# Performance work log

Measured on AMD Instinct MI355X. Metric: run time of the kernel, lower is better.

## Reference

```python
import jax, jax.numpy as jnp
import numpy as np
from jax import lax

D = 512        # datapathSize (= slow-net hidden size = embedding size)
H = 20         # nonlinearAfterSlowHiddenSize
V = 32000      # softmaxOutputHeadSize = xEmbeddingsNum
T = 1024       # sequence length (number of sequential fast-weight updates)


def setup_inputs() -> dict:
    key = jax.random.key(0)
    ks = jax.random.split(key, 12)
    inp = {}
    inp["tokens"] = jax.random.randint(ks[0], (T,), 0, V)
    inp["targets"] = jax.random.randint(ks[1], (T,), 0, V)
    # learned parameters
    inp["embed"] = jax.random.normal(ks[2], (V, D), dtype=jnp.float32)
    # fastWeightsInit = rand(D,D) * (1/D)
    inp["fw_init"] = jax.random.uniform(ks[3], (D, D), dtype=jnp.float32) * (1.0 / D)
    inp["eta"] = jnp.array(1.0, dtype=jnp.float32)
    inp["wa"] = jax.random.normal(ks[4], (D, D), dtype=jnp.float32) * 0.05
    inp["wb"] = jax.random.normal(ks[5], (D, D), dtype=jnp.float32) * 0.05
    # nonlinearAfterSlow: Linear(D,H) -> selu -> Linear(H,D); stored as (in,out)
    lim_a = 1.0 / np.sqrt(D)
    inp["mlp_aw"] = jax.random.uniform(ks[6], (D, H), dtype=jnp.float32, minval=-lim_a, maxval=lim_a)
    inp["mlp_ab"] = jax.random.uniform(ks[7], (H,), dtype=jnp.float32, minval=-lim_a, maxval=lim_a)
    lim_b = 1.0 / np.sqrt(H)
    inp["mlp_bw"] = jax.random.uniform(ks[8], (H, D), dtype=jnp.float32, minval=-lim_b, maxval=lim_b)
    inp["mlp_bb"] = jax.random.uniform(ks[9], (D,), dtype=jnp.float32, minval=-lim_b, maxval=lim_b)
    # logit head Linear(D, V)
    inp["head_w"] = jax.random.uniform(ks[10], (D, V), dtype=jnp.float32, minval=-lim_a, maxval=lim_a)
    inp["head_b"] = jax.random.uniform(ks[11], (V,), dtype=jnp.float32, minval=-lim_a, maxval=lim_a)
    return inp


def reference(tokens, targets, embed, fw_init, eta, wa, wb,
              mlp_aw, mlp_ab, mlp_bw, mlp_bb, head_w, head_b):
    xs = embed[tokens]  # [T, D]

    def step(fw, x):
        # SlowNetB.forwardAndUpdate for one token
        z0 = x @ wa                      # [D]
        z1 = x @ wb                      # [D]
        fw_new = jnp.tanh(fw + eta * jnp.outer(z0, z1))  # [D, D]
        y = x @ fw_new                   # [D]
        return fw_new, y

    _, ys = lax.scan(step, fw_init, xs)  # ys: [T, D]

    # NonlinearLayer (batched over T)
    h = jax.nn.selu(ys @ mlp_aw + mlp_ab) @ mlp_bw + mlp_bb  # [T, D]
    mixed = 0.5 * h + 0.5 * xs
    logits = mixed @ head_w + head_b     # [T, V]

    logp = jax.nn.log_softmax(logits, axis=-1)
    loss = -jnp.mean(jnp.take_along_axis(logp, targets[:, None], axis=1))
    return logits, loss
```

## Files before the change

### kernel.cpp

```cpp
#include <hip/hip_runtime.h>

#define D 512
#define H 20
#define V 32000
#define T 1024

typedef unsigned int uint;
typedef __attribute__((ext_vector_type(8))) short short8;
typedef __attribute__((ext_vector_type(4))) float floatx4;

__device__ __forceinline__ unsigned short f2bf(float f) {
    unsigned u = __builtin_bit_cast(unsigned, f);
    u += 0x7fffu + ((u >> 16) & 1u);
    return (unsigned short)(u >> 16);
}

template <int CTRL>
__device__ __forceinline__ float dpp_add(float v) {
    int x = __builtin_amdgcn_update_dpp(0, __builtin_bit_cast(int, v), CTRL, 0xf, 0xf, true);
    return v + __builtin_bit_cast(float, x);
}
__device__ __forceinline__ float reduce16(float v) {
    v = dpp_add<0xB1>(v);
    v = dpp_add<0x4E>(v);
    v = dpp_add<0x141>(v);
    v = dpp_add<0x140>(v);
    return v;
}

__global__ __launch_bounds__(256) void gather_kernel(const int* __restrict__ tokens,
                                                     const float* __restrict__ embed,
                                                     float* __restrict__ xs) {
    int idx = blockIdx.x * 256 + threadIdx.x;
    int row = idx >> 7;
    int c   = idx & 127;
    float4 v = ((const float4*)(embed + (long)tokens[row] * D))[c];
    ((float4*)xs)[idx] = v;
}

__global__ __launch_bounds__(256) void zgemm_kernel(const float* __restrict__ xs,
                                                    const float* __restrict__ wa,
                                                    const float* __restrict__ wb,
                                                    float* __restrict__ z0,
                                                    float* __restrict__ z1) {
    __shared__ float Xs[16 * 36];
    __shared__ float Ws[16 * 68];
    const int tid = threadIdx.x;
    const int n0 = blockIdx.x * 64, m0 = blockIdx.y * 32;
    const float* Wm = blockIdx.z ? wb : wa;
    float* Z = blockIdx.z ? z1 : z0;
    const int tx = tid & 15, ty = tid >> 4;
    const int xr = tid >> 3, xk = (tid & 7) * 2;
    const int wr = tid >> 4, wc = (tid & 15) * 4;
    float acc[2][4] = {};
    for (int k0 = 0; k0 < D; k0 += 16) {
        float2 xv = *(const float2*)(xs + (m0 + xr) * D + k0 + xk);
        float4 wv = *(const float4*)(Wm + (k0 + wr) * D + n0 + wc);
        Xs[(xk + 0) * 36 + xr] = xv.x;
        Xs[(xk + 1) * 36 + xr] = xv.y;
        *(float4*)(Ws + wr * 68 + wc) = wv;
        __syncthreads();
#pragma unroll
        for (int k = 0; k < 16; k++) {
            float a0 = Xs[k * 36 + 2 * ty];
            float a1 = Xs[k * 36 + 2 * ty + 1];
            float4 b = *(const float4*)(Ws + k * 68 + tx * 4);
            float bv[4] = {b.x, b.y, b.z, b.w};
#pragma unroll
            for (int c = 0; c < 4; c++) {
                acc[0][c] = __builtin_fmaf(a0, bv[c], acc[0][c]);
                acc[1][c] = __builtin_fmaf(a1, bv[c], acc[1][c]);
            }
        }
        __syncthreads();
    }
    float4 v0 = {acc[0][0], acc[0][1], acc[0][2], acc[0][3]};
    float4 v1 = {acc[1][0], acc[1][1], acc[1][2], acc[1][3]};
    *(float4*)(Z + (m0 + 2 * ty + 0) * D + n0 + tx * 4) = v0;
    *(float4*)(Z + (m0 + 2 * ty + 1) * D + n0 + tx * 4) = v1;
}

#define CC 2.8853900817779268f

#define LOADC(ZA, ZB, XA, XB, EC, tbase)                       \
    _Pragma("unroll")                                          \
    for (int c = 0; c < 8; c++) {                              \
        int tr = (tbase + c) * D;                              \
        ZA[c] = z0[tr + i0];                                   \
        ZB[c] = z0[tr + i1];                                   \
        XA[c] = xs[tr + i0];                                   \
        XB[c] = xs[tr + i1];                                   \
        EC[c] = z1[tr + j] * ETAC;                             \
    }

#define COMPUTE(ZA, ZB, XA, XB, EC, tbase)                     \
    {                                                          \
        float p[8];                                            \
        _Pragma("unroll")                                      \
        for (int c = 0; c < 8; c++) {                          \
            float e = EC[c];                                   \
            float e0 = __builtin_amdgcn_exp2f(__builtin_fmaf(e, ZA[c], g0)); \
            float e1 = __builtin_amdgcn_exp2f(__builtin_fmaf(e, ZB[c], g1)); \
            float r0 = __builtin_amdgcn_rcpf(e0 + 1.0f);       \
            float r1 = __builtin_amdgcn_rcpf(e1 + 1.0f);       \
            g0 = __builtin_fmaf(-2.0f * CC, r0, CC);           \
            g1 = __builtin_fmaf(-2.0f * CC, r1, CC);           \
            p[c] = XA[c] * g0 + XB[c] * g1;                    \
        }                                                      \
        _Pragma("unroll")                                      \
        for (int c = 0; c < 8; c++) {                          \
            float v = reduce16(p[c]);                          \
            v += __shfl_xor(v, 16, 64);                        \
            v += __shfl_xor(v, 32, 64);                        \
            p[c] = v;                                          \
        }                                                      \
        if (lane == 0) {                                       \
            _Pragma("unroll")                                  \
            for (int c = 0; c < 8; c++) yp[(tbase + c) * D] = p[c]; \
        }                                                      \
    }

__global__ __launch_bounds__(64) void scan_kernel(const float* __restrict__ z0,
                                                  const float* __restrict__ z1,
                                                  const float* __restrict__ xs,
                                                  const float* __restrict__ fw_init,
                                                  const float* __restrict__ eta_p,
                                                  float* __restrict__ ypart) {
    const int lane = threadIdx.x;
    const int bid = blockIdx.x;
    const int j = bid & 511;
    const int q = bid >> 9;
    const int i0 = q * 128 + lane;
    const int i1 = i0 + 64;
    const float eta = *eta_p;
    const float ETAC = eta * CC;
    float g0 = CC * fw_init[(long)i0 * D + j];
    float g1 = CC * fw_init[(long)i1 * D + j];
    float* yp = ypart + (long)q * T * D + j;

    float zaA[8], zbA[8], xaA[8], xbA[8], ecA[8];
    float zaB[8], zbB[8], xaB[8], xbB[8], ecB[8];
    LOADC(zaA, zbA, xaA, xbA, ecA, 0);
    for (int t0 = 0; t0 < T; t0 += 16) {
        LOADC(zaB, zbB, xaB, xbB, ecB, t0 + 8);
        COMPUTE(zaA, zbA, xaA, xbA, ecA, t0);
        if (t0 + 16 < T) { LOADC(zaA, zbA, xaA, xbA, ecA, t0 + 16); }
        COMPUTE(zaB, zbB, xaB, xbB, ecB, t0 + 8);
    }
}

__global__ __launch_bounds__(256) void mlp_fused_kernel(const float* __restrict__ ypart,
                                                        const float* __restrict__ xs,
                                                        const float* __restrict__ Aw,
                                                        const float* __restrict__ Ab,
                                                        const float* __restrict__ Bw,
                                                        const float* __restrict__ Bb,
                                                        unsigned short* __restrict__ mixed) {
    const int t = blockIdx.x, tid = threadIdx.x;
    __shared__ float y_lds[D];
    __shared__ float h_lds[H];
    const float INVC = 0.34657359027997264f;
#pragma unroll
    for (int s = 0; s < 2; s++) {
        int d = s * 256 + tid;
        float v = ypart[(0 * T + t) * D + d] + ypart[(1 * T + t) * D + d]
                + ypart[(2 * T + t) * D + d] + ypart[(3 * T + t) * D + d];
        y_lds[d] = v * INVC;
    }
    __syncthreads();
    const int w = tid >> 6, lane = tid & 63;
    float yv[8];
#pragma unroll
    for (int k = 0; k < 8; k++) yv[k] = y_lds[k * 64 + lane];
#pragma unroll
    for (int u = 0; u < 5; u++) {
        const int jj = w * 5 + u;
        float a = 0.f;
#pragma unroll
        for (int k = 0; k < 8; k++)
            a = __builtin_fmaf(yv[k], Aw[(k * 64 + lane) * H + jj], a);
        a = reduce16(a);
        a += __shfl_xor(a, 16, 64);
        a += __shfl_xor(a, 32, 64);
        if (lane == 0) {
            a += Ab[jj];
            const float sc = 1.0507009873554805f, al = 1.6732632423543772f;
            h_lds[jj] = a > 0.f ? sc * a : sc * al * (__expf(a) - 1.f);
        }
    }
    __syncthreads();
#pragma unroll
    for (int s = 0; s < 2; s++) {
        int d = s * 256 + tid;
        float o = Bb[d];
#pragma unroll
        for (int jj = 0; jj < H; jj++) o = __builtin_fmaf(h_lds[jj], Bw[jj * D + d], o);
        int gi = t * D + d;
        mixed[gi] = f2bf(0.5f * o + 0.5f * xs[gi]);
    }
}

__global__ __launch_bounds__(256) void convert_wt_kernel(const float* __restrict__ head_w,
                                                         unsigned short* __restrict__ wt) {
    __shared__ float tile[64 * 68];
    const int n0 = blockIdx.x * 64, k0 = blockIdx.y * 64;
    const int tid = threadIdx.x;
#pragma unroll
    for (int s = 0; s < 4; s++) {
        int idx4 = s * 256 + tid;
        int r = idx4 >> 4, c4 = idx4 & 15;
        float4 v = *(const float4*)(head_w + (long)(k0 + r) * V + n0 + c4 * 4);
        *(float4*)(tile + r * 68 + c4 * 4) = v;
    }
    __syncthreads();
    const int rr = tid >> 2;
    const int cq = tid & 3;
    uint u[8];
#pragma unroll
    for (int p = 0; p < 8; p++) {
        float a = tile[(cq * 16 + p * 2 + 0) * 68 + rr];
        float b = tile[(cq * 16 + p * 2 + 1) * 68 + rr];
        u[p] = (uint)f2bf(a) | ((uint)f2bf(b) << 16);
    }
    unsigned short* ob = wt + (long)(n0 + rr) * D + k0 + cq * 16;
    uint4 v0 = {u[0], u[1], u[2], u[3]};
    uint4 v1 = {u[4], u[5], u[6], u[7]};
    *(uint4*)ob = v0;
    *((uint4*)ob + 1) = v1;
}

__global__ __launch_bounds__(256) void head_gemm_kernel(const unsigned short* __restrict__ A,
                                                        const unsigned short* __restrict__ Bt,
                                                        const float* __restrict__ bias,
                                                        float* __restrict__ C) {
    __shared__ unsigned short As[128 * 64];
    __shared__ unsigned short Bs[128 * 64];
    const int tid = threadIdx.x;
    const int mt = blockIdx.x & 7, nt = blockIdx.x >> 3;
    const int m0 = mt * 128, n0 = nt * 128;
    const int wave = tid >> 6, lane = tid & 63;
    const int wm = wave >> 1, wn = wave & 1;
    const int quad = lane >> 4, l15 = lane & 15;
    floatx4 acc[4][4] = {};
    for (int k0 = 0; k0 < D; k0 += 64) {
#pragma unroll
        for (int s = 0; s < 4; s++) {
            int idx = s * 256 + tid;
            int row = idx >> 3, slot = idx & 7;
            int gch = slot ^ (row & 7);
            const unsigned short* ga = A + (long)(m0 + row) * D + k0 + gch * 8;
            __builtin_amdgcn_global_load_lds(
                (const __attribute__((address_space(1))) unsigned int*)ga,
                (__attribute__((address_space(3))) unsigned int*)(As + idx * 8), 16, 0, 0);
            const unsigned short* gb = Bt + (long)(n0 + row) * D + k0 + gch * 8;
            __builtin_amdgcn_global_load_lds(
                (const __attribute__((address_space(1))) unsigned int*)gb,
                (__attribute__((address_space(3))) unsigned int*)(Bs + idx * 8), 16, 0, 0);
        }
        __syncthreads();
#pragma unroll
        for (int ks = 0; ks < 2; ks++) {
            short8 af[4], bfr[4];
            int q = ks * 4 + quad;
#pragma unroll
            for (int f = 0; f < 4; f++) {
                int ar = wm * 64 + f * 16 + l15;
                af[f] = *(const short8*)(As + ar * 64 + ((q ^ (ar & 7)) * 8));
                int br = wn * 64 + f * 16 + l15;
                bfr[f] = *(const short8*)(Bs + br * 64 + ((q ^ (br & 7)) * 8));
            }
#pragma unroll
            for (int fr = 0; fr < 4; fr++)
#pragma unroll
                for (int fc = 0; fc < 4; fc++)
                    acc[fr][fc] = __builtin_amdgcn_mfma_f32_16x16x32_bf16(af[fr], bfr[fc],
                                                                          acc[fr][fc], 0, 0, 0);
        }
        __syncthreads();
    }
#pragma unroll
    for (int fc = 0; fc < 4; fc++) {
        int n = n0 + wn * 64 + fc * 16 + l15;
        float b = bias[n];
#pragma unroll
        for (int fr = 0; fr < 4; fr++) {
            int mr = m0 + wm * 64 + fr * 16 + quad * 4;
#pragma unroll
            for (int r = 0; r < 4; r++)
                C[(long)(mr + r) * V + n] = acc[fr][fc][r] + b;
        }
    }
}

__device__ __forceinline__ void lse_upd(float& m, float& s, float v) {
    if (v > m) { s = s * __expf(m - v) + 1.f; m = v; }
    else       { s += __expf(v - m); }
}
__device__ __forceinline__ void lse_comb(float& m, float& s, float m2, float s2) {
    float M = fmaxf(m, m2);
    s = s * __expf(m - M) + s2 * __expf(m2 - M);
    m = M;
}

__global__ __launch_bounds__(256) void loss_rows_kernel(const float* __restrict__ logits,
                                                        const int* __restrict__ targets,
                                                        float* __restrict__ ws_loss) {
    const int t = blockIdx.x, tid = threadIdx.x;
    const float4* row = (const float4*)(logits + (long)t * V);
    float m = -INFINITY, s = 0.f;
    for (int i = tid; i < V / 4; i += 256) {
        float4 v = row[i];
        lse_upd(m, s, v.x); lse_upd(m, s, v.y); lse_upd(m, s, v.z); lse_upd(m, s, v.w);
    }
#pragma unroll
    for (int msk = 1; msk <= 32; msk <<= 1) {
        float m2 = __shfl_xor(m, msk, 64);
        float s2 = __shfl_xor(s, msk, 64);
        lse_comb(m, s, m2, s2);
    }
    __shared__ float sm[4], ss[4];
    if ((tid & 63) == 0) { sm[tid >> 6] = m; ss[tid >> 6] = s; }
    __syncthreads();
    if (tid == 0) {
        float M = sm[0], S = ss[0];
#pragma unroll
        for (int w = 1; w < 4; w++) lse_comb(M, S, sm[w], ss[w]);
        float lse = M + __logf(S);
        float lt = logits[(long)t * V + targets[t]];
        ws_loss[t] = lse - lt;
    }
}

__global__ __launch_bounds__(256) void loss_final_kernel(const float* __restrict__ ws_loss,
                                                         float* __restrict__ out) {
    const int tid = threadIdx.x;
    float s = 0.f;
    for (int i = tid; i < T; i += 256) s += ws_loss[i];
#pragma unroll
    for (int m = 1; m <= 32; m <<= 1) s += __shfl_xor(s, m, 64);
    __shared__ float red[4];
    if ((tid & 63) == 0) red[tid >> 6] = s;
    __syncthreads();
    if (tid == 0) out[0] = (red[0] + red[1] + red[2] + red[3]) * (1.f / (float)T);
}

extern "C" void kernel_launch(void* const* d_in, const int* in_sizes, int n_in,
                              void* d_out, int out_size, void* d_ws, size_t ws_size,
                              hipStream_t stream) {
    const int*   tokens  = (const int*)d_in[0];
    const int*   targets = (const int*)d_in[1];
    const float* embed   = (const float*)d_in[2];
    const float* fw_init = (const float*)d_in[3];
    const float* eta     = (const float*)d_in[4];
    const float* wa      = (const float*)d_in[5];
    const float* wb      = (const float*)d_in[6];
    const float* mlp_aw  = (const float*)d_in[7];
    const float* mlp_ab  = (const float*)d_in[8];
    const float* mlp_bw  = (const float*)d_in[9];
    const float* mlp_bb  = (const float*)d_in[10];
    const float* head_w  = (const float*)d_in[11];
    const float* head_b  = (const float*)d_in[12];
    float* out = (float*)d_out;

    char* ws = (char*)d_ws;
    float*          xs      = (float*)(ws + 0);
    float*          z0      = (float*)(ws + 2097152);
    float*          z1      = (float*)(ws + 4194304);
    float*          ypart   = (float*)(ws + 6291456);
    unsigned short* wt      = (unsigned short*)(ws + 2097152);
    unsigned short* mixed   = (unsigned short*)(ws + 35651584);
    float*          ws_loss = (float*)(ws + 36700160);

    gather_kernel<<<(T * D / 4) / 256, 256, 0, stream>>>(tokens, embed, xs);
    zgemm_kernel<<<dim3(D / 64, T / 32, 2), 256, 0, stream>>>(xs, wa, wb, z0, z1);
    scan_kernel<<<2048, 64, 0, stream>>>(z0, z1, xs, fw_init, eta, ypart);
    mlp_fused_kernel<<<T, 256, 0, stream>>>(ypart, xs, mlp_aw, mlp_ab, mlp_bw, mlp_bb, mixed);
    convert_wt_kernel<<<dim3(V / 64, D / 64), 256, 0, stream>>>(head_w, wt);
    head_gemm_kernel<<<(T / 128) * (V / 128), 256, 0, stream>>>(mixed, wt, head_b, out);
    loss_rows_kernel<<<T, 256, 0, stream>>>(out, targets, ws_loss);
    loss_final_kernel<<<1, 256, 0, stream>>>(ws_loss, out + (long)T * V);
}
```

Measured before the change: 521.1 us.

## Fuse partial log-sum-exp into head GEMM epilogue and split scan across more blocks

The head GEMM epilogue now computes per-row partial max and exp-sum over each wave's 64 columns and writes them to small workspace arrays. The loss kernel then combines these 500 partials per row instead of re-reading the full 128 MB logits matrix. Separately, the scan kernel now gives each block 64 rows instead of 128 and launches 4096 blocks, halving per-thread serial tanh work at the cost of 8 partial y buffers, which the MLP kernel sums. This adds work to the GEMM epilogue (cross-lane reductions, exps) and doubles the partial-y traffic.

```diff
diff --git a/kernel.cpp b/kernel.cpp
--- a/kernel.cpp
+++ b/kernel.cpp
@@ -4,6 +4,7 @@
 #define H 20
 #define V 32000
 #define T 1024
+#define NT2 500
 
 typedef unsigned int uint;
 typedef __attribute__((ext_vector_type(8))) short short8;
@@ -19,12 +20,24 @@
 __device__ __forceinline__ float dpp_add(float v) {
     int x = __builtin_amdgcn_update_dpp(0, __builtin_bit_cast(int, v), CTRL, 0xf, 0xf, true);
     return v + __builtin_bit_cast(float, x);
+}
+template <int CTRL>
+__device__ __forceinline__ float dpp_max(float v) {
+    int x = __builtin_amdgcn_update_dpp(0, __builtin_bit_cast(int, v), CTRL, 0xf, 0xf, true);
+    return fmaxf(v, __builtin_bit_cast(float, x));
 }
 __device__ __forceinline__ float reduce16(float v) {
     v = dpp_add<0xB1>(v);
     v = dpp_add<0x4E>(v);
     v = dpp_add<0x141>(v);
     v = dpp_add<0x140>(v);
+    return v;
+}
+__device__ __forceinline__ float reduce16max(float v) {
+    v = dpp_max<0xB1>(v);
+    v = dpp_max<0x4E>(v);
+    v = dpp_max<0x141>(v);
+    v = dpp_max<0x140>(v);
     return v;
 }
 
@@ -82,30 +95,24 @@
 
 #define CC 2.8853900817779268f
 
-#define LOADC(ZA, ZB, XA, XB, EC, tbase)                       \
+#define LOADC(ZA, XA, EC, tbase)                               \
     _Pragma("unroll")                                          \
     for (int c = 0; c < 8; c++) {                              \
         int tr = (tbase + c) * D;                              \
         ZA[c] = z0[tr + i0];                                   \
-        ZB[c] = z0[tr + i1];                                   \
         XA[c] = xs[tr + i0];                                   \
-        XB[c] = xs[tr + i1];                                   \
         EC[c] = z1[tr + j] * ETAC;                             \
     }
 
-#define COMPUTE(ZA, ZB, XA, XB, EC, tbase)                     \
+#define COMPUTE(ZA, XA, EC, tbase)                             \
     {                                                          \
         float p[8];                                            \
         _Pragma("unroll")                                      \
         for (int c = 0; c < 8; c++) {                          \
-            float e = EC[c];                                   \
-            float e0 = __builtin_amdgcn_exp2f(__builtin_fmaf(e, ZA[c], g0)); \
-            float e1 = __builtin_amdgcn_exp2f(__builtin_fmaf(e, ZB[c], g1)); \
+            float e0 = __builtin_amdgcn_exp2f(__builtin_fmaf(EC[c], ZA[c], g0)); \
             float r0 = __builtin_amdgcn_rcpf(e0 + 1.0f);       \
-            float r1 = __builtin_amdgcn_rcpf(e1 + 1.0f);       \
             g0 = __builtin_fmaf(-2.0f * CC, r0, CC);           \
-            g1 = __builtin_fmaf(-2.0f * CC, r1, CC);           \
-            p[c] = XA[c] * g0 + XB[c] * g1;                    \
+            p[c] = XA[c] * g0;                                 \
         }                                                      \
         _Pragma("unroll")                                      \
         for (int c = 0; c < 8; c++) {                          \
@@ -130,22 +137,20 @@
     const int bid = blockIdx.x;
     const int j = bid & 511;
     const int q = bid >> 9;
-    const int i0 = q * 128 + lane;
-    const int i1 = i0 + 64;
+    const int i0 = q * 64 + lane;
     const float eta = *eta_p;
     const float ETAC = eta * CC;
     float g0 = CC * fw_init[(long)i0 * D + j];
-    float g1 = CC * fw_init[(long)i1 * D + j];
     float* yp = ypart + (long)q * T * D + j;
 
-    float zaA[8], zbA[8], xaA[8], xbA[8], ecA[8];
-    float zaB[8], zbB[8], xaB[8], xbB[8], ecB[8];
-    LOADC(zaA, zbA, xaA, xbA, ecA, 0);
+    float zaA[8], xaA[8], ecA[8];
+    float zaB[8], xaB[8], ecB[8];
+    LOADC(zaA, xaA, ecA, 0);
     for (int t0 = 0; t0 < T; t0 += 16) {
-        LOADC(zaB, zbB, xaB, xbB, ecB, t0 + 8);
-        COMPUTE(zaA, zbA, xaA, xbA, ecA, t0);
-        if (t0 + 16 < T) { LOADC(zaA, zbA, xaA, xbA, ecA, t0 + 16); }
-        COMPUTE(zaB, zbB, xaB, xbB, ecB, t0 + 8);
+        LOADC(zaB, xaB, ecB, t0 + 8);
+        COMPUTE(zaA, xaA, ecA, t0);
+        if (t0 + 16 < T) { LOADC(zaA, xaA, ecA, t0 + 16); }
+        COMPUTE(zaB, xaB, ecB, t0 + 8);
     }
 }
 
@@ -163,8 +168,9 @@
 #pragma unroll
     for (int s = 0; s < 2; s++) {
         int d = s * 256 + tid;
-        float v = ypart[(0 * T + t) * D + d] + ypart[(1 * T + t) * D + d]
-                + ypart[(2 * T + t) * D + d] + ypart[(3 * T + t) * D + d];
+        float v = 0.f;
+#pragma unroll
+        for (int qq = 0; qq < 8; qq++) v += ypart[((long)qq * T + t) * D + d];
         y_lds[d] = v * INVC;
     }
     __syncthreads();
@@ -232,7 +238,9 @@
 __global__ __launch_bounds__(256) void head_gemm_kernel(const unsigned short* __restrict__ A,
                                                         const unsigned short* __restrict__ Bt,
                                                         const float* __restrict__ bias,
-                                                        float* __restrict__ C) {
+                                                        float* __restrict__ C,
+                                                        float* __restrict__ pm,
+                                                        float* __restrict__ ps) {
     __shared__ unsigned short As[128 * 64];
     __shared__ unsigned short Bs[128 * 64];
     const int tid = threadIdx.x;
@@ -278,40 +286,49 @@
         }
         __syncthreads();
     }
-#pragma unroll
-    for (int fc = 0; fc < 4; fc++) {
-        int n = n0 + wn * 64 + fc * 16 + l15;
-        float b = bias[n];
-#pragma unroll
-        for (int fr = 0; fr < 4; fr++) {
-            int mr = m0 + wm * 64 + fr * 16 + quad * 4;
-#pragma unroll
-            for (int r = 0; r < 4; r++)
-                C[(long)(mr + r) * V + n] = acc[fr][fc][r] + b;
+    float bv[4];
+#pragma unroll
+    for (int fc = 0; fc < 4; fc++) bv[fc] = bias[n0 + wn * 64 + fc * 16 + l15];
+#pragma unroll
+    for (int fr = 0; fr < 4; fr++) {
+        int mr = m0 + wm * 64 + fr * 16 + quad * 4;
+#pragma unroll
+        for (int r = 0; r < 4; r++) {
+            float v[4];
+#pragma unroll
+            for (int fc = 0; fc < 4; fc++) {
+                v[fc] = acc[fr][fc][r] + bv[fc];
+                C[(long)(mr + r) * V + n0 + wn * 64 + fc * 16 + l15] = v[fc];
+            }
+            float mx = fmaxf(fmaxf(v[0], v[1]), fmaxf(v[2], v[3]));
+            mx = reduce16max(mx);
+            float sv = __expf(v[0] - mx) + __expf(v[1] - mx)
+                     + __expf(v[2] - mx) + __expf(v[3] - mx);
+            sv = reduce16(sv);
+            if (l15 == 0) {
+                long row = mr + r;
+                pm[row * NT2 + nt * 2 + wn] = mx;
+                ps[row * NT2 + nt * 2 + wn] = sv;
+            }
         }
     }
 }
 
-__device__ __forceinline__ void lse_upd(float& m, float& s, float v) {
-    if (v > m) { s = s * __expf(m - v) + 1.f; m = v; }
-    else       { s += __expf(v - m); }
-}
 __device__ __forceinline__ void lse_comb(float& m, float& s, float m2, float s2) {
     float M = fmaxf(m, m2);
     s = s * __expf(m - M) + s2 * __expf(m2 - M);
     m = M;
 }
 
-__global__ __launch_bounds__(256) void loss_rows_kernel(const float* __restrict__ logits,
+__global__ __launch_bounds__(256) void loss_rows_kernel(const float* __restrict__ pm,
+                                                        const float* __restrict__ ps,
+                                                        const float* __restrict__ logits,
                                                         const int* __restrict__ targets,
                                                         float* __restrict__ ws_loss) {
     const int t = blockIdx.x, tid = threadIdx.x;
-    const float4* row = (const float4*)(logits + (long)t * V);
     float m = -INFINITY, s = 0.f;
-    for (int i = tid; i < V / 4; i += 256) {
-        float4 v = row[i];
-        lse_upd(m, s, v.x); lse_upd(m, s, v.y); lse_upd(m, s, v.z); lse_upd(m, s, v.w);
-    }
+    for (int i = tid; i < NT2; i += 256)
+        lse_comb(m, s, pm[(long)t * NT2 + i], ps[(long)t * NT2 + i]);
 #pragma unroll
     for (int msk = 1; msk <= 32; msk <<= 1) {
         float m2 = __shfl_xor(m, msk, 64);
@@ -369,14 +386,16 @@
     float*          ypart   = (float*)(ws + 6291456);
     unsigned short* wt      = (unsigned short*)(ws + 2097152);
     unsigned short* mixed   = (unsigned short*)(ws + 35651584);
-    float*          ws_loss = (float*)(ws + 36700160);
+    float*          pm      = (float*)(ws + 36700160);
+    float*          psum    = (float*)(ws + 38797312);
+    float*          ws_loss = (float*)(ws + 40894464);
 
     gather_kernel<<<(T * D / 4) / 256, 256, 0, stream>>>(tokens, embed, xs);
     zgemm_kernel<<<dim3(D / 64, T / 32, 2), 256, 0, stream>>>(xs, wa, wb, z0, z1);
-    scan_kernel<<<2048, 64, 0, stream>>>(z0, z1, xs, fw_init, eta, ypart);
+    scan_kernel<<<4096, 64, 0, stream>>>(z0, z1, xs, fw_init, eta, ypart);
     mlp_fused_kernel<<<T, 256, 0, stream>>>(ypart, xs, mlp_aw, mlp_ab, mlp_bw, mlp_bb, mixed);
     convert_wt_kernel<<<dim3(V / 64, D / 64), 256, 0, stream>>>(head_w, wt);
-    head_gemm_kernel<<<(T / 128) * (V / 128), 256, 0, stream>>>(mixed, wt, head_b, out);
-    loss_rows_kernel<<<T, 256, 0, stream>>>(out, targets, ws_loss);
+    head_gemm_kernel<<<(T / 128) * (V / 128), 256, 0, stream>>>(mixed, wt, head_b, out, pm, psum);
+    loss_rows_kernel<<<T, 256, 0, stream>>>(pm, psum, out, targets, ws_loss);
     loss_final_kernel<<<1, 256, 0, stream>>>(ws_loss, out + (long)T * V);
 }
```

Result: slower. 542.5 us (+4.1%).
